# Kernel optimization log

Hardware: AMD Instinct MI355X
Metric: run time of the kernel (lower is better)

## Reference

```python
import jax, jax.numpy as jnp
import numpy as np

N = 50000  # num nodes

def _cheb_norm(edge_index, n):
    # PyG ChebConv sym normalization with default lambda_max=2.0:
    # scaled Laplacian L_hat = -D^{-1/2} A D^{-1/2} (diagonal cancels to 0)
    src, dst = edge_index[0], edge_index[1]
    deg = jax.ops.segment_sum(jnp.ones(src.shape[0], jnp.float32), src, num_segments=n)
    dinv = jnp.where(deg > 0, jax.lax.rsqrt(jnp.maximum(deg, 1.0)), 0.0)
    norm = -dinv[src] * dinv[dst]  # [E]
    return src, dst, norm

def _prop(x, src, dst, norm, n):
    # out[i] = sum_{(j->i)} norm_e * x[j]
    return jax.ops.segment_sum(norm[:, None] * x[src], dst, num_segments=n)

def _cheb_layer(x, src, dst, norm, W, b, n):
    # W: [K=3, in, out]; Tx0=x, Tx1=L_hat x, Tx2=2 L_hat Tx1 - Tx0
    tx0 = x
    tx1 = _prop(tx0, src, dst, norm, n)
    tx2 = 2.0 * _prop(tx1, src, dst, norm, n) - tx0
    return tx0 @ W[0] + tx1 @ W[1] + tx2 @ W[2] + b

def setup_inputs() -> dict:
    key = jax.random.key(0)
    ks = jax.random.split(key, 8)
    E = 800000
    v = jax.random.normal(ks[0], (N, 32), jnp.float32)
    edge_index = jax.random.randint(ks[1], (2, E), 0, N, dtype=jnp.int64)
    def glorot(k, shape):
        fan_in, fan_out = shape[1], shape[2]
        s = jnp.sqrt(6.0 / (fan_in + fan_out))
        return jax.random.uniform(k, shape, jnp.float32, -s, s)
    W1 = glorot(ks[2], (3, 32, 128));  b1 = jnp.zeros((128,), jnp.float32)
    W2 = glorot(ks[3], (3, 128, 256)); b2 = jnp.zeros((256,), jnp.float32)
    W3 = glorot(ks[4], (3, 256, 512)); b3 = jnp.zeros((512,), jnp.float32)
    return {"v": v, "edge_index": edge_index, "W1": W1, "b1": b1,
            "W2": W2, "b2": b2, "W3": W3, "b3": b3}

def reference(v, edge_index, W1, b1, W2, b2, W3, b3):
    n = v.shape[0]
    src, dst, norm = _cheb_norm(edge_index, n)
    x = jax.nn.relu(_cheb_layer(v, src, dst, norm, W1, b1, n))
    x = jax.nn.relu(_cheb_layer(x, src, dst, norm, W2, b2, n))
    x = jax.nn.relu(_cheb_layer(x, src, dst, norm, W3, b3, n))
    return x
```

## Files before the change

kernel.cpp:

```cpp
#include <hip/hip_runtime.h>
#include <hip/hip_bf16.h>


typedef __bf16 bf16x8 __attribute__((ext_vector_type(8)));
typedef float f32x4 __attribute__((ext_vector_type(4)));
typedef unsigned short ushort_t;

struct EdgeRec { int s; float w; };

__device__ inline float bf2f(ushort_t u) { return __builtin_bit_cast(float, (unsigned)u << 16); }
__device__ inline ushort_t f2bf(float f) { return __builtin_bit_cast(ushort_t, (__bf16)f); }

union U8 { int4 v; ushort_t u[8]; };

__device__ inline void gload16(const ushort_t* g, ushort_t* l) {
    __builtin_amdgcn_global_load_lds(
        (const __attribute__((address_space(1))) unsigned int*)g,
        (__attribute__((address_space(3))) unsigned int*)l, 16, 0, 0);
}

__global__ void count_kernel(const int* __restrict__ src, const int* __restrict__ dst,
                             int* __restrict__ cnt_src, int* __restrict__ cnt_dst, int E, int N) {
    int e = blockIdx.x * blockDim.x + threadIdx.x;
    if (e >= E) return;
    int s = src[e], d = dst[e];
    if ((unsigned)s < (unsigned)N) atomicAdd(&cnt_src[s], 1);
    if ((unsigned)d < (unsigned)N) atomicAdd(&cnt_dst[d], 1);
}

__global__ void dinv_kernel(const int* __restrict__ cnt_src, float* __restrict__ dinv, int N) {
    int i = blockIdx.x * blockDim.x + threadIdx.x;
    if (i >= N) return;
    int c = cnt_src[i];
    dinv[i] = (c > 0) ? rsqrtf((float)c) : 0.0f;
}

__global__ void blocksum_kernel(const int* __restrict__ cnt, int* __restrict__ bsum, int N) {
    int i = blockIdx.x * 256 + threadIdx.x;
    int v = (i < N) ? cnt[i] : 0;
#pragma unroll
    for (int off = 32; off >= 1; off >>= 1) v += __shfl_xor(v, off);
    __shared__ int ws[4];
    if ((threadIdx.x & 63) == 0) ws[threadIdx.x >> 6] = v;
    __syncthreads();
    if (threadIdx.x == 0) bsum[blockIdx.x] = ws[0] + ws[1] + ws[2] + ws[3];
}

__global__ void scanblock_kernel(const int* __restrict__ bsum, int* __restrict__ boff, int nb) {
    __shared__ int s[256];
    int t = threadIdx.x;
    int v = (t < nb) ? bsum[t] : 0;
    s[t] = v;
    __syncthreads();
#pragma unroll
    for (int off = 1; off < 256; off <<= 1) {
        int u = (t >= off) ? s[t - off] : 0;
        __syncthreads();
        s[t] += u;
        __syncthreads();
    }
    if (t < nb) boff[t] = s[t] - v;
}

__global__ void scatter_scan_kernel(const int* __restrict__ cnt, const int* __restrict__ boff,
                                    int* __restrict__ row_ptr, int* __restrict__ wofs, int N) {
    __shared__ int s[256];
    int t = threadIdx.x;
    int i = blockIdx.x * 256 + t;
    int v = (i < N) ? cnt[i] : 0;
    s[t] = v;
    __syncthreads();
#pragma unroll
    for (int off = 1; off < 256; off <<= 1) {
        int u = (t >= off) ? s[t - off] : 0;
        __syncthreads();
        s[t] += u;
        __syncthreads();
    }
    int run = boff[blockIdx.x] + s[t] - v;
    if (i < N) { row_ptr[i] = run; wofs[i] = run; }
    else if (i == N) row_ptr[N] = run;
}

__global__ void fill_kernel(const int* __restrict__ src, const int* __restrict__ dst,
                            const float* __restrict__ dinv, int* __restrict__ wofs,
                            EdgeRec* __restrict__ ep, int E, int N) {
    int e = blockIdx.x * blockDim.x + threadIdx.x;
    if (e >= E) return;
    int s = src[e], d = dst[e];
    if ((unsigned)s >= (unsigned)N || (unsigned)d >= (unsigned)N) return;
    int pos = atomicAdd(&wofs[d], 1);
    EdgeRec er; er.s = s; er.w = -dinv[s] * dinv[d];
    ep[pos] = er;
}

__global__ void convin_kernel(const float* __restrict__ v, ushort_t* __restrict__ txb, int N) {
    int id = blockIdx.x * blockDim.x + threadIdx.x;
    if (id >= N * 4) return;
    int node = id >> 2, c = (id & 3) << 3;
    const float* p = &v[(size_t)node * 32 + c];
    U8 o;
#pragma unroll
    for (int i = 0; i < 8; ++i) o.u[i] = f2bf(p[i]);
    *(int4*)&txb[(size_t)node * 96 + c] = o.v;
}

template <int F, int PASS>
__global__ __launch_bounds__(256) void prop_kernel(ushort_t* __restrict__ txb,
                                                   const int* __restrict__ row_ptr,
                                                   const EdgeRec* __restrict__ ep, int N) {
    constexpr int T = F / 8;
    constexpr int NPB = 256 / T;
    constexpr int RS = 3 * F;
    constexpr int SRC = (PASS == 1) ? 0 : F;
    int tf = threadIdx.x % T;
    int node = blockIdx.x * NPB + threadIdx.x / T;
    if (node >= N) return;
    int e0 = row_ptr[node], e1 = row_ptr[node + 1];
    int fo = tf * 8;
    float acc[8] = {};
    int e = e0;
    for (; e + 3 < e1; e += 4) {
        EdgeRec er[4];
        U8 x[4];
#pragma unroll
        for (int j = 0; j < 4; ++j) er[j] = ep[e + j];
#pragma unroll
        for (int j = 0; j < 4; ++j)
            x[j].v = *(const int4*)&txb[(size_t)er[j].s * RS + SRC + fo];
#pragma unroll
        for (int j = 0; j < 4; ++j)
#pragma unroll
            for (int i = 0; i < 8; ++i) acc[i] += er[j].w * bf2f(x[j].u[i]);
    }
    for (; e < e1; ++e) {
        EdgeRec ea = ep[e];
        U8 xa;
        xa.v = *(const int4*)&txb[(size_t)ea.s * RS + SRC + fo];
#pragma unroll
        for (int i = 0; i < 8; ++i) acc[i] += ea.w * bf2f(xa.u[i]);
    }
    U8 o;
    if (PASS == 1) {
#pragma unroll
        for (int i = 0; i < 8; ++i) o.u[i] = f2bf(acc[i]);
        *(int4*)&txb[(size_t)node * RS + F + fo] = o.v;
    } else {
        U8 x0;
        x0.v = *(const int4*)&txb[(size_t)node * RS + fo];
#pragma unroll
        for (int i = 0; i < 8; ++i) o.u[i] = f2bf(2.f * acc[i] - bf2f(x0.u[i]));
        *(int4*)&txb[(size_t)node * RS + 2 * F + fo] = o.v;
    }
}

__global__ void convw_kernel(const float* __restrict__ W, ushort_t* __restrict__ Wt, int K, int Nout) {
    int id = blockIdx.x * blockDim.x + threadIdx.x;
    if (id >= K * Nout) return;
    int n = id / K, k = id % K;
    Wt[id] = f2bf(W[(size_t)k * Nout + n]);
}

template <bool BF16OUT, int NY>
__global__ __launch_bounds__(256, 3) void gemm_kernel(const ushort_t* __restrict__ A,
                                                      const ushort_t* __restrict__ Bt,
                                                      const float* __restrict__ bias,
                                                      void* __restrict__ outp,
                                                      int M, int K, int Nout, int ostride,
                                                      int nwg) {
    __shared__ ushort_t As[2][128 * 32];
    __shared__ ushort_t Bs[2][128 * 32];
    int tid = threadIdx.x;
    int orig = blockIdx.x;
    int q = nwg >> 3, r = nwg & 7;
    int xcd = orig & 7, m8 = orig >> 3;
    int t = (xcd < r ? xcd * (q + 1) : r * (q + 1) + (xcd - r) * q) + m8;
    int brow = (t / NY) * 128;
    int bcol = (t % NY) * 128;

    int lane = tid & 63, w = tid >> 6;
    int wr = w >> 1, wc = w & 1;
    int g = lane >> 4, lr = lane & 15;
    f32x4 acc[4][4] = {};

    int srow[2], scol[2];
#pragma unroll
    for (int p = 0; p < 2; ++p) {
        int row = (p * 4 + w) * 16 + (lane >> 2);
        srow[p] = row;
        scol[p] = ((lane & 3) ^ ((row >> 1) & 3)) * 8;
    }

    size_t abase[2], bbase[2];
#pragma unroll
    for (int p = 0; p < 2; ++p) {
        int ar = brow + srow[p]; ar = ar < M ? ar : M - 1;
        abase[p] = (size_t)ar * K + scol[p];
        bbase[p] = (size_t)(bcol + srow[p]) * K + scol[p];
    }

    auto stage = [&](int buf, int kt) {
#pragma unroll
        for (int p = 0; p < 2; ++p) {
            gload16(&A[abase[p] + kt], &As[buf][(p * 4 + w) * 512]);
            gload16(&Bt[bbase[p] + kt], &Bs[buf][(p * 4 + w) * 512]);
        }
    };

    int aoff[4], boff4[4];
#pragma unroll
    for (int m = 0; m < 4; ++m) {
        int row = wr * 64 + m * 16 + lr;
        aoff[m] = row * 32 + ((g ^ ((row >> 1) & 3)) * 8);
    }
#pragma unroll
    for (int n = 0; n < 4; ++n) {
        int row = wc * 64 + n * 16 + lr;
        boff4[n] = row * 32 + ((g ^ ((row >> 1) & 3)) * 8);
    }

    stage(0, 0);
    int cur = 0;
    for (int kt = 0; kt < K; kt += 32) {
        if (kt + 32 < K) {
            stage(cur ^ 1, kt + 32);
            asm volatile("s_waitcnt vmcnt(4)" ::: "memory");
        } else {
            asm volatile("s_waitcnt vmcnt(0)" ::: "memory");
        }
        __builtin_amdgcn_s_barrier();
        bf16x8 a[4], b[4];
#pragma unroll
        for (int m = 0; m < 4; ++m) a[m] = *(const bf16x8*)&As[cur][aoff[m]];
#pragma unroll
        for (int n = 0; n < 4; ++n) b[n] = *(const bf16x8*)&Bs[cur][boff4[n]];
#pragma unroll
        for (int m = 0; m < 4; ++m)
#pragma unroll
            for (int n = 0; n < 4; ++n)
                acc[m][n] = __builtin_amdgcn_mfma_f32_16x16x32_bf16(a[m], b[n], acc[m][n], 0, 0, 0);
        __builtin_amdgcn_s_barrier();
        cur ^= 1;
    }

#pragma unroll
    for (int m = 0; m < 4; ++m) {
        int grow_base = brow + wr * 64 + m * 16 + g * 4;
#pragma unroll
        for (int n = 0; n < 4; ++n) {
            int gcol = bcol + wc * 64 + n * 16 + lr;
            float bv = bias[gcol];
#pragma unroll
            for (int r2 = 0; r2 < 4; ++r2) {
                int grow = grow_base + r2;
                if (grow < M) {
                    float v2 = acc[m][n][r2] + bv;
                    v2 = v2 > 0.f ? v2 : 0.f;
                    if (BF16OUT)
                        ((ushort_t*)outp)[(size_t)grow * ostride + gcol] = f2bf(v2);
                    else
                        ((float*)outp)[(size_t)grow * ostride + gcol] = v2;
                }
            }
        }
    }
}

extern "C" void kernel_launch(void* const* d_in, const int* in_sizes, int n_in,
                              void* d_out, int out_size, void* d_ws, size_t ws_size,
                              hipStream_t stream) {
    const float* v  = (const float*)d_in[0];
    const int*   ei = (const int*)d_in[1];
    const float* W1 = (const float*)d_in[2];
    const float* b1 = (const float*)d_in[3];
    const float* W2 = (const float*)d_in[4];
    const float* b2 = (const float*)d_in[5];
    const float* W3 = (const float*)d_in[6];
    const float* b3 = (const float*)d_in[7];

    const int N = in_sizes[0] / 32;
    const int E = in_sizes[1] / 2;
    const int* src = ei;
    const int* dst = ei + E;

    char* ws = (char*)d_ws;
    size_t off = 0;
    auto alloc = [&](size_t bytes) {
        off = (off + 255) & ~(size_t)255;
        char* p = ws + off;
        off += bytes;
        return p;
    };
    EdgeRec*  ep      = (EdgeRec*)alloc((size_t)E * 8);
    int*      row_ptr = (int*)alloc((size_t)(N + 1) * 4);
    int*      wofs    = (int*)alloc((size_t)N * 4);
    int*      cnt_src = (int*)alloc((size_t)N * 4);
    int*      cnt_dst = (int*)alloc((size_t)N * 4);
    float*    dinv    = (float*)alloc((size_t)N * 4);
    int*      bsum    = (int*)alloc((size_t)256 * 4);
    int*      boff    = (int*)alloc((size_t)256 * 4);
    ushort_t* Wt      = (ushort_t*)alloc((size_t)512 * 768 * 2);
    ushort_t* txb3    = (ushort_t*)alloc((size_t)N * 768 * 2);
    ushort_t* txb1    = txb3;
    ushort_t* txb2    = (ushort_t*)d_out;
    float*    outF    = (float*)d_out;

    const int nb = (N + 255) / 256;

    hipMemsetAsync(cnt_src, 0, (size_t)N * 4, stream);
    hipMemsetAsync(cnt_dst, 0, (size_t)N * 4, stream);
    count_kernel<<<(E + 255) / 256, 256, 0, stream>>>(src, dst, cnt_src, cnt_dst, E, N);
    dinv_kernel<<<(N + 255) / 256, 256, 0, stream>>>(cnt_src, dinv, N);
    blocksum_kernel<<<nb, 256, 0, stream>>>(cnt_dst, bsum, N);
    scanblock_kernel<<<1, 256, 0, stream>>>(bsum, boff, nb);
    scatter_scan_kernel<<<nb, 256, 0, stream>>>(cnt_dst, boff, row_ptr, wofs, N);
    fill_kernel<<<(E + 255) / 256, 256, 0, stream>>>(src, dst, dinv, wofs, ep, E, N);

    const int mt = (N + 127) / 128;

    convin_kernel<<<(N * 4 + 255) / 256, 256, 0, stream>>>(v, txb1, N);
    prop_kernel<32, 1><<<(N + 63) / 64, 256, 0, stream>>>(txb1, row_ptr, ep, N);
    prop_kernel<32, 2><<<(N + 63) / 64, 256, 0, stream>>>(txb1, row_ptr, ep, N);
    convw_kernel<<<(96 * 128 + 255) / 256, 256, 0, stream>>>(W1, Wt, 96, 128);
    gemm_kernel<true, 1><<<mt * 1, 256, 0, stream>>>(txb1, Wt, b1, txb2, N, 96, 128, 384, mt * 1);

    prop_kernel<128, 1><<<(N + 15) / 16, 256, 0, stream>>>(txb2, row_ptr, ep, N);
    prop_kernel<128, 2><<<(N + 15) / 16, 256, 0, stream>>>(txb2, row_ptr, ep, N);
    convw_kernel<<<(384 * 256 + 255) / 256, 256, 0, stream>>>(W2, Wt, 384, 256);
    gemm_kernel<true, 2><<<mt * 2, 256, 0, stream>>>(txb2, Wt, b2, txb3, N, 384, 256, 768, mt * 2);

    prop_kernel<256, 1><<<(N + 7) / 8, 256, 0, stream>>>(txb3, row_ptr, ep, N);
    prop_kernel<256, 2><<<(N + 7) / 8, 256, 0, stream>>>(txb3, row_ptr, ep, N);
    convw_kernel<<<(768 * 512 + 255) / 256, 256, 0, stream>>>(W3, Wt, 768, 512);
    gemm_kernel<false, 4><<<mt * 4, 256, 0, stream>>>(txb3, Wt, b3, outF, N, 768, 512, 512, mt * 4);
}
```

Baseline: 453.6 us.

## Fold Chebyshev recurrence into weights and software-pipeline edge loads in propagation

Pass 2 of the propagation now stores the raw L_hat·Tx1 instead of 2·L_hat·Tx1 − Tx0. The weight conversion compensates by folding the algebra into the weights: W0−W2 for the Tx0 block, W1 unchanged, and 2·W2 for the third block. This drops one feature read per node from pass 2. The edge loop is restructured to prefetch the next batch of edge records while the current batch's gathers run, padding the tail with zero weights. GEMM launch bounds rise to 4 waves per SIMD, which may cause register spills. The folded weights are rounded to bf16, which slightly changes numerics.

After: 443.3 us. 1.02x faster.

```diff
diff --git a/kernel.cpp b/kernel.cpp
--- a/kernel.cpp
+++ b/kernel.cpp
@@ -109,6 +109,7 @@
 __global__ __launch_bounds__(256) void prop_kernel(ushort_t* __restrict__ txb,
                                                    const int* __restrict__ row_ptr,
                                                    const EdgeRec* __restrict__ ep, int N) {
+    constexpr int U = 4;
     constexpr int T = F / 8;
     constexpr int NPB = 256 / T;
     constexpr int RS = 3 * F;
@@ -119,50 +120,61 @@
     int e0 = row_ptr[node], e1 = row_ptr[node + 1];
     int fo = tf * 8;
     float acc[8] = {};
-    int e = e0;
-    for (; e + 3 < e1; e += 4) {
-        EdgeRec er[4];
-        U8 x[4];
-#pragma unroll
-        for (int j = 0; j < 4; ++j) er[j] = ep[e + j];
-#pragma unroll
-        for (int j = 0; j < 4; ++j)
-            x[j].v = *(const int4*)&txb[(size_t)er[j].s * RS + SRC + fo];
-#pragma unroll
-        for (int j = 0; j < 4; ++j)
-#pragma unroll
-            for (int i = 0; i < 8; ++i) acc[i] += er[j].w * bf2f(x[j].u[i]);
-    }
-    for (; e < e1; ++e) {
-        EdgeRec ea = ep[e];
-        U8 xa;
-        xa.v = *(const int4*)&txb[(size_t)ea.s * RS + SRC + fo];
-#pragma unroll
-        for (int i = 0; i < 8; ++i) acc[i] += ea.w * bf2f(xa.u[i]);
+    int deg = e1 - e0;
+    if (deg > 0) {
+        int nbatch = (deg + U - 1) / U;
+        EdgeRec cur[U], nxt[U];
+#pragma unroll
+        for (int j = 0; j < U; ++j) {
+            int ei = e0 + j;
+            EdgeRec rr = ep[ei < e1 ? ei : e1 - 1];
+            if (ei >= e1) rr.w = 0.f;
+            cur[j] = rr;
+        }
+        for (int b = 0; b < nbatch; ++b) {
+            U8 x[U];
+#pragma unroll
+            for (int j = 0; j < U; ++j)
+                x[j].v = *(const int4*)&txb[(size_t)cur[j].s * RS + SRC + fo];
+            if (b + 1 < nbatch) {
+                int nbase = e0 + (b + 1) * U;
+#pragma unroll
+                for (int j = 0; j < U; ++j) {
+                    int ei = nbase + j;
+                    EdgeRec rr = ep[ei < e1 ? ei : e1 - 1];
+                    if (ei >= e1) rr.w = 0.f;
+                    nxt[j] = rr;
+                }
+            }
+#pragma unroll
+            for (int j = 0; j < U; ++j)
+#pragma unroll
+                for (int i = 0; i < 8; ++i) acc[i] += cur[j].w * bf2f(x[j].u[i]);
+#pragma unroll
+            for (int j = 0; j < U; ++j) cur[j] = nxt[j];
+        }
     }
     U8 o;
-    if (PASS == 1) {
-#pragma unroll
-        for (int i = 0; i < 8; ++i) o.u[i] = f2bf(acc[i]);
-        *(int4*)&txb[(size_t)node * RS + F + fo] = o.v;
-    } else {
-        U8 x0;
-        x0.v = *(const int4*)&txb[(size_t)node * RS + fo];
-#pragma unroll
-        for (int i = 0; i < 8; ++i) o.u[i] = f2bf(2.f * acc[i] - bf2f(x0.u[i]));
-        *(int4*)&txb[(size_t)node * RS + 2 * F + fo] = o.v;
-    }
-}
-
-__global__ void convw_kernel(const float* __restrict__ W, ushort_t* __restrict__ Wt, int K, int Nout) {
+#pragma unroll
+    for (int i = 0; i < 8; ++i) o.u[i] = f2bf(acc[i]);
+    *(int4*)&txb[(size_t)node * RS + (PASS == 1 ? F : 2 * F) + fo] = o.v;
+}
+
+__global__ void convw_kernel(const float* __restrict__ W, ushort_t* __restrict__ Wt,
+                             int F, int Nout) {
+    int K = 3 * F;
     int id = blockIdx.x * blockDim.x + threadIdx.x;
     if (id >= K * Nout) return;
     int n = id / K, k = id % K;
-    Wt[id] = f2bf(W[(size_t)k * Nout + n]);
+    float val;
+    if (k < F)            val = W[(size_t)k * Nout + n] - W[(size_t)(2 * F + k) * Nout + n];
+    else if (k < 2 * F)   val = W[(size_t)k * Nout + n];
+    else                  val = 2.0f * W[(size_t)k * Nout + n];
+    Wt[id] = f2bf(val);
 }
 
 template <bool BF16OUT, int NY>
-__global__ __launch_bounds__(256, 3) void gemm_kernel(const ushort_t* __restrict__ A,
+__global__ __launch_bounds__(256, 4) void gemm_kernel(const ushort_t* __restrict__ A,
                                                       const ushort_t* __restrict__ Bt,
                                                       const float* __restrict__ bias,
                                                       void* __restrict__ outp,
@@ -321,16 +333,16 @@
     convin_kernel<<<(N * 4 + 255) / 256, 256, 0, stream>>>(v, txb1, N);
     prop_kernel<32, 1><<<(N + 63) / 64, 256, 0, stream>>>(txb1, row_ptr, ep, N);
     prop_kernel<32, 2><<<(N + 63) / 64, 256, 0, stream>>>(txb1, row_ptr, ep, N);
-    convw_kernel<<<(96 * 128 + 255) / 256, 256, 0, stream>>>(W1, Wt, 96, 128);
+    convw_kernel<<<(96 * 128 + 255) / 256, 256, 0, stream>>>(W1, Wt, 32, 128);
     gemm_kernel<true, 1><<<mt * 1, 256, 0, stream>>>(txb1, Wt, b1, txb2, N, 96, 128, 384, mt * 1);
 
     prop_kernel<128, 1><<<(N + 15) / 16, 256, 0, stream>>>(txb2, row_ptr, ep, N);
     prop_kernel<128, 2><<<(N + 15) / 16, 256, 0, stream>>>(txb2, row_ptr, ep, N);
-    convw_kernel<<<(384 * 256 + 255) / 256, 256, 0, stream>>>(W2, Wt, 384, 256);
+    convw_kernel<<<(384 * 256 + 255) / 256, 256, 0, stream>>>(W2, Wt, 128, 256);
     gemm_kernel<true, 2><<<mt * 2, 256, 0, stream>>>(txb2, Wt, b2, txb3, N, 384, 256, 768, mt * 2);
 
     prop_kernel<256, 1><<<(N + 7) / 8, 256, 0, stream>>>(txb3, row_ptr, ep, N);
     prop_kernel<256, 2><<<(N + 7) / 8, 256, 0, stream>>>(txb3, row_ptr, ep, N);
-    convw_kernel<<<(768 * 512 + 255) / 256, 256, 0, stream>>>(W3, Wt, 768, 512);
+    convw_kernel<<<(768 * 512 + 255) / 256, 256, 0, stream>>>(W3, Wt, 256, 512);
     gemm_kernel<false, 4><<<mt * 4, 256, 0, stream>>>(txb3, Wt, b3, outF, N, 768, 512, 512, mt * 4);
 }
```
